# Optimization experiments

Hardware: AMD Instinct MI355X
Metric: run time of the kernel (lower is better)

## Reference

```python
import jax, jax.numpy as jnp
import numpy as np

N = 100000   # nodes
E = 1600000  # edges
G = 2048     # graphs in batch
NC = 204     # n_classes
DEPTH = 5
EPS = 1e-5


def setup_inputs() -> dict:
    key = jax.random.key(0)
    ks = jax.random.split(key, 20)
    rn = lambda k, s, sc=0.05: (jax.random.normal(k, s, jnp.float32) * sc)
    inp = {
        "h": jax.random.normal(ks[0], (N, 78), jnp.float32),
        "edge_src": jax.random.randint(ks[1], (E,), 0, N),
        "edge_dst": jax.random.randint(ks[2], (E,), 0, N),
        "graph_ids": jnp.sort(jax.random.randint(ks[3], (N,), 0, G)),
        "W1": rn(ks[4], (78, 128)),
        "b1": rn(ks[5], (128,)),
        "g1_gamma": jnp.ones((128,), jnp.float32),
        "g1_beta": jnp.zeros((128,), jnp.float32),
        "Wg": rn(ks[6], (DEPTH - 1, 128, 128)),
        "bg": rn(ks[7], (DEPTH - 1, 128)),
        "g_gamma": jnp.ones((DEPTH - 1, 128), jnp.float32),
        "g_beta": jnp.zeros((DEPTH - 1, 128), jnp.float32),
        "fc1_W": rn(ks[8], (128, 512)),
        "fc1_b": rn(ks[9], (512,)),
        "bn1_gamma": jnp.ones((512,), jnp.float32),
        "bn1_beta": jnp.zeros((512,), jnp.float32),
        "lin_W": rn(ks[10], (512, 256)),
        "lin_b": rn(ks[11], (256,)),
        "lbn_gamma": jnp.ones((256,), jnp.float32),
        "lbn_beta": jnp.zeros((256,), jnp.float32),
        "fc2_W": rn(ks[12], (256, 408)),
        "fc2_b": rn(ks[13], (408,)),
    }
    return inp


def _bn(x, gamma, beta):
    # torch BatchNorm1d training-mode normalization: biased batch var, eps=1e-5
    mu = jnp.mean(x, axis=0)
    var = jnp.var(x, axis=0)
    return (x - mu) * jax.lax.rsqrt(var + EPS) * gamma + beta


def _gin(h, src, dst, W, b):
    # DGL GINConv (eps=0, sum agg): apply_func(h + sum_neigh(h)); module adds apply_func(h)
    agg = jax.ops.segment_sum(h[src], dst, num_segments=h.shape[0])  # [N, d]
    return (h + agg) @ W + b + (h @ W + b)


def reference(h, edge_src, edge_dst, graph_ids, W1, b1, g1_gamma, g1_beta,
              Wg, bg, g_gamma, g_beta, fc1_W, fc1_b, bn1_gamma, bn1_beta,
              lin_W, lin_b, lbn_gamma, lbn_beta, fc2_W, fc2_b):
    x = jax.nn.relu(_bn(_gin(h, edge_src, edge_dst, W1, b1), g1_gamma, g1_beta))
    for i in range(DEPTH - 1):
        x = jax.nn.relu(_bn(_gin(x, edge_src, edge_dst, Wg[i], bg[i]),
                            g_gamma[i], g_beta[i]))
    # sum readout over nodes of each graph -> [G, 128]
    xg = jax.ops.segment_sum(x, graph_ids, num_segments=G)
    x = jax.nn.relu(_bn(xg @ fc1_W + fc1_b, bn1_gamma, bn1_beta))
    x = jax.nn.relu(_bn(x @ lin_W + lin_b, lbn_gamma, lbn_beta))
    logits = x @ fc2_W + fc2_b          # [G, 2*NC]
    return jax.nn.sigmoid(logits[:, -NC:])  # [G, NC]
```

## Files before the change

kernel.cpp:

```cpp
#include <hip/hip_runtime.h>
#include <hip/hip_bf16.h>
#include <math.h>

#define N_NODES 100000
#define N_EDGES 1600000
#define N_GRAPHS 2048
#define NCLS 204
#define EPS_BN 1e-5f
#define NBUCK ((N_NODES + 255) / 256)
#define BIN_CHUNK 8192

typedef __attribute__((ext_vector_type(8))) short short8;
typedef __attribute__((ext_vector_type(4))) float f32x4;

__device__ __forceinline__ float bf_lo(uint v) { union { uint i; float f; } c; c.i = v << 16; return c.f; }
__device__ __forceinline__ float bf_hi(uint v) { union { uint i; float f; } c; c.i = v & 0xffff0000u; return c.f; }
__device__ __forceinline__ ushort f2bf(float v) {
  __hip_bfloat16 b = __float2bfloat16(v);
  return *reinterpret_cast<ushort*>(&b);
}
__device__ __forceinline__ uint pack2(float a, float b) {
  return (uint)f2bf(a) | ((uint)f2bf(b) << 16);
}

__global__ __launch_bounds__(256) void k_bin_count(const int* __restrict__ dst,
                                                   int* __restrict__ bcnt, int E) {
  __shared__ int hist[NBUCK];
  int t = threadIdx.x;
  int e0 = blockIdx.x * BIN_CHUNK;
  for (int b = t; b < NBUCK; b += 256) hist[b] = 0;
  __syncthreads();
  for (int e = e0 + t; e < min(e0 + BIN_CHUNK, E); e += 256)
    atomicAdd(&hist[dst[e] >> 8], 1);
  __syncthreads();
  for (int b = t; b < NBUCK; b += 256)
    if (hist[b] > 0) atomicAdd(&bcnt[b], hist[b]);
}

__global__ __launch_bounds__(512) void k_bucket_scan(const int* __restrict__ bcnt,
                                                     int* __restrict__ bbase,
                                                     int* __restrict__ bcur) {
  __shared__ int sh[512];
  int t = threadIdx.x;
  int v = (t < NBUCK) ? bcnt[t] : 0;
  sh[t] = v;
  __syncthreads();
  for (int d = 1; d < 512; d <<= 1) {
    int x = (t >= d) ? sh[t - d] : 0;
    __syncthreads();
    sh[t] += x;
    __syncthreads();
  }
  if (t < NBUCK) {
    bbase[t + 1] = sh[t];
    bcur[t] = sh[t] - v;
    if (t == 0) bbase[0] = 0;
  }
}

__global__ __launch_bounds__(256) void k_bin(const int* __restrict__ src,
                                             const int* __restrict__ dst,
                                             int* __restrict__ cursor,
                                             uint* __restrict__ staging, int E) {
  __shared__ int hist[NBUCK];
  __shared__ int base_s[NBUCK];
  int t = threadIdx.x;
  int e0 = blockIdx.x * BIN_CHUNK;
  for (int b = t; b < NBUCK; b += 256) hist[b] = 0;
  __syncthreads();
  for (int e = e0 + t; e < min(e0 + BIN_CHUNK, E); e += 256)
    atomicAdd(&hist[dst[e] >> 8], 1);
  __syncthreads();
  for (int b = t; b < NBUCK; b += 256) {
    int hh = hist[b];
    if (hh > 0) base_s[b] = atomicAdd(&cursor[b], hh);
    hist[b] = 0;
  }
  __syncthreads();
  for (int e = e0 + t; e < min(e0 + BIN_CHUNK, E); e += 256) {
    int d = dst[e];
    int b = d >> 8;
    int r = atomicAdd(&hist[b], 1);
    staging[base_s[b] + r] = (uint)src[e] | ((uint)(d & 255) << 24);
  }
}

__global__ __launch_bounds__(256) void k_place2(const uint* __restrict__ staging,
                                                const int* __restrict__ bbase,
                                                int* __restrict__ row_ptr,
                                                int* __restrict__ csr, int nNodes, int E) {
  __shared__ int cnt[256];
  __shared__ int scn[256];
  __shared__ int cur[256];
  int t = threadIdx.x;
  int b = blockIdx.x;
  int n0 = b * 256;
  cnt[t] = 0;
  __syncthreads();
  int s = bbase[b], e = bbase[b + 1];
  for (int i = s + t; i < e; i += 256) atomicAdd(&cnt[staging[i] >> 24], 1);
  __syncthreads();
  int v = cnt[t];
  scn[t] = v;
  __syncthreads();
  for (int d = 1; d < 256; d <<= 1) {
    int x = (t >= d) ? scn[t - d] : 0;
    __syncthreads();
    scn[t] += x;
    __syncthreads();
  }
  int excl = scn[t] - v;
  if (n0 + t < nNodes) row_ptr[n0 + t] = s + excl;
  cur[t] = s + excl;
  __syncthreads();
  for (int i = s + t; i < e; i += 256) {
    uint ed = staging[i];
    int pos = atomicAdd(&cur[ed >> 24], 1);
    csr[pos] = (int)(ed & 0xFFFFFF);
  }
  if (b == 0 && t == 0) row_ptr[nNodes] = E;
}

__global__ void k_conv_h(const float* __restrict__ h, uint* __restrict__ hb, int nNodes) {
  int i = blockIdx.x * blockDim.x + threadIdx.x;
  if (i < nNodes * 64) {
    int n = i >> 6, cp = i & 63;
    int c = cp * 2;
    float a = (c < 78) ? h[(size_t)n * 78 + c] : 0.0f;
    float b = (c + 1 < 78) ? h[(size_t)n * 78 + c + 1] : 0.0f;
    hb[i] = pack2(a, b);
  }
}

__global__ void k_prep_wt_all(const float* __restrict__ W1, const float* __restrict__ Wg,
                              ushort* __restrict__ Wt) {
  int i = blockIdx.x * blockDim.x + threadIdx.x;
  int layer = blockIdx.y;
  if (i < 128 * 128) {
    int n = i >> 7, k = i & 127;
    const float* W = (layer == 0) ? W1 : Wg + (size_t)(layer - 1) * 128 * 128;
    int K = (layer == 0) ? 78 : 128;
    float v = (k < K) ? W[(size_t)k * 128 + n] : 0.0f;
    Wt[(size_t)layer * 128 * 128 + i] = f2bf(v);
  }
}

__global__ void k_prep_wt_gen(const float* __restrict__ W, int wld, int col_off, int nkeep,
                              int K, ushort* __restrict__ Wt, int total) {
  int i = blockIdx.x * blockDim.x + threadIdx.x;
  if (i < total) {
    int n = i / K, k = i - n * K;
    float v = (n < nkeep) ? W[(size_t)k * wld + col_off + n] : 0.0f;
    Wt[i] = f2bf(v);
  }
}

template <bool NRM>
__global__ __launch_bounds__(256) void k_agg_f(const uint* __restrict__ y,
                                               const int* __restrict__ row_ptr,
                                               const int* __restrict__ csr,
                                               const float* __restrict__ psum,
                                               const float* __restrict__ psq,
                                               const float* __restrict__ pgamma,
                                               const float* __restrict__ pbeta,
                                               float invM,
                                               uint* __restrict__ M, int nNodes) {
  int n = blockIdx.x * 4 + (threadIdx.x >> 6);
  if (n >= nNodes) return;
  int l = threadIdx.x & 63;
  float A0 = 1.f, B0 = 0.f, A1 = 1.f, B1 = 0.f;
  if (NRM) {
    int c0 = 2 * l, c1 = 2 * l + 1;
    float mu0 = psum[c0] * invM;
    float va0 = psq[c0] * invM - mu0 * mu0;
    A0 = pgamma[c0] * rsqrtf(va0 + EPS_BN);
    B0 = pbeta[c0] - mu0 * A0;
    float mu1 = psum[c1] * invM;
    float va1 = psq[c1] * invM - mu1 * mu1;
    A1 = pgamma[c1] * rsqrtf(va1 + EPS_BN);
    B1 = pbeta[c1] - mu1 * A1;
  }
  auto flo = [&](uint v) { float x = bf_lo(v); return NRM ? fmaxf(x * A0 + B0, 0.f) : x; };
  auto fhi = [&](uint v) { float x = bf_hi(v); return NRM ? fmaxf(x * A1 + B1, 0.f) : x; };

  uint self = y[(size_t)n * 64 + l];
  float a0 = 2.0f * flo(self);
  float a1 = 2.0f * fhi(self);
  int s = row_ptr[n], e = row_ptr[n + 1];

  for (int base = s; base < e; base += 64) {
    int cnt = e - base;
    if (cnt > 64) cnt = 64;
    int myidx = (base + l < e) ? csr[base + l] : 0;
    int j = 0;
    for (; j + 4 <= cnt; j += 4) {
      int i0 = __shfl(myidx, j);
      int i1 = __shfl(myidx, j + 1);
      int i2 = __shfl(myidx, j + 2);
      int i3 = __shfl(myidx, j + 3);
      uint v0 = y[(size_t)i0 * 64 + l];
      uint v1 = y[(size_t)i1 * 64 + l];
      uint v2 = y[(size_t)i2 * 64 + l];
      uint v3 = y[(size_t)i3 * 64 + l];
      a0 += flo(v0) + flo(v1) + flo(v2) + flo(v3);
      a1 += fhi(v0) + fhi(v1) + fhi(v2) + fhi(v3);
    }
    for (; j < cnt; j++) {
      int i0 = __shfl(myidx, j);
      uint v = y[(size_t)i0 * 64 + l];
      a0 += flo(v);
      a1 += fhi(v);
    }
  }
  M[(size_t)n * 64 + l] = pack2(a0, a1);
}

#define SWZ(row, boff) ((boff) ^ (((row) & 7) << 4))
__global__ __launch_bounds__(256) void k_gemm_mfma(const ushort* __restrict__ A,
                                                   const ushort* __restrict__ Wt,
                                                   const float* __restrict__ bias, float bscale,
                                                   ushort* __restrict__ Y, int Mrows,
                                                   float* __restrict__ gsum,
                                                   float* __restrict__ gsq) {
  __shared__ ushort As[128 * 128];
  __shared__ ushort Bs[128 * 128];
  __shared__ float sred[4][128], qred[4][128];
  int t = threadIdx.x;
  int r0 = blockIdx.x * 128;
  char* Ab = (char*)As;
  char* Bb = (char*)Bs;

  for (int it = 0; it < 8; it++) {
    int e = it * 256 + t;
    int row = e >> 4, seg = e & 15;
    uint4 va = make_uint4(0, 0, 0, 0);
    int gr = r0 + row;
    if (gr < Mrows) va = *reinterpret_cast<const uint4*>(A + (size_t)gr * 128 + seg * 8);
    *reinterpret_cast<uint4*>(Ab + row * 256 + SWZ(row, seg * 16)) = va;
    uint4 vb = *reinterpret_cast<const uint4*>(Wt + (size_t)row * 128 + seg * 8);
    *reinterpret_cast<uint4*>(Bb + row * 256 + SWZ(row, seg * 16)) = vb;
  }
  __syncthreads();

  int wi = t >> 6;
  int l = t & 63;
  int lr = l & 15;
  int kp = l >> 4;

  f32x4 acc[2][8];
#pragma unroll
  for (int mi = 0; mi < 2; mi++)
#pragma unroll
    for (int ni = 0; ni < 8; ni++) acc[mi][ni] = (f32x4){0.f, 0.f, 0.f, 0.f};

#pragma unroll
  for (int ki = 0; ki < 4; ki++) {
    short8 a[2], b[8];
#pragma unroll
    for (int mi = 0; mi < 2; mi++) {
      int row = wi * 32 + mi * 16 + lr;
      a[mi] = *reinterpret_cast<const short8*>(Ab + row * 256 + SWZ(row, ki * 64 + kp * 16));
    }
#pragma unroll
    for (int ni = 0; ni < 8; ni++) {
      int row = ni * 16 + lr;
      b[ni] = *reinterpret_cast<const short8*>(Bb + row * 256 + SWZ(row, ki * 64 + kp * 16));
    }
#pragma unroll
    for (int mi = 0; mi < 2; mi++)
#pragma unroll
      for (int ni = 0; ni < 8; ni++)
        acc[mi][ni] = __builtin_amdgcn_mfma_f32_16x16x32_bf16(a[mi], b[ni], acc[mi][ni], 0, 0, 0);
  }

  float s_part[8], q_part[8];
#pragma unroll
  for (int ni = 0; ni < 8; ni++) { s_part[ni] = 0.f; q_part[ni] = 0.f; }

#pragma unroll
  for (int mi = 0; mi < 2; mi++) {
    int rbase = r0 + wi * 32 + mi * 16 + kp * 4;
#pragma unroll
    for (int ni = 0; ni < 8; ni++) {
      int col = ni * 16 + lr;
      float bb = bscale * bias[col];
#pragma unroll
      for (int j = 0; j < 4; j++) {
        int r = rbase + j;
        if (r < Mrows) {
          float yv = acc[mi][ni][j] + bb;
          Y[(size_t)r * 128 + col] = f2bf(yv);
          s_part[ni] += yv;
          q_part[ni] += yv * yv;
        }
      }
    }
  }

#pragma unroll
  for (int ni = 0; ni < 8; ni++) {
    s_part[ni] += __shfl_xor(s_part[ni], 16, 64);
    s_part[ni] += __shfl_xor(s_part[ni], 32, 64);
    q_part[ni] += __shfl_xor(q_part[ni], 16, 64);
    q_part[ni] += __shfl_xor(q_part[ni], 32, 64);
  }
  if (kp == 0) {
#pragma unroll
    for (int ni = 0; ni < 8; ni++) {
      sred[wi][ni * 16 + lr] = s_part[ni];
      qred[wi][ni * 16 + lr] = q_part[ni];
    }
  }
  __syncthreads();
  if (t < 128) {
    float S = sred[0][t] + sred[1][t] + sred[2][t] + sred[3][t];
    float Q = qred[0][t] + qred[1][t] + qred[2][t] + qred[3][t];
    atomicAdd(&gsum[t], S);
    atomicAdd(&gsq[t], Q);
  }
}

template <int AMODE, int OMODE>
__global__ __launch_bounds__(256) void k_head_mfma(const void* __restrict__ Aptr,
                                                   int Mrows, int K,
                                                   const ushort* __restrict__ Wt,
                                                   const float* __restrict__ bias,
                                                   int col_off, int ncols,
                                                   const float* __restrict__ nAc,
                                                   const float* __restrict__ nBc,
                                                   void* __restrict__ Yout, int Nld,
                                                   float* __restrict__ gsum,
                                                   float* __restrict__ gsq) {
  __shared__ ushort As[128 * 128];
  __shared__ ushort Bs[128 * 128];
  __shared__ float sred[4][128], qred[4][128];
  int t = threadIdx.x;
  int r0 = blockIdx.y * 128;
  int c0 = blockIdx.x * 128;
  char* Ab = (char*)As;
  char* Bb = (char*)Bs;

  int wi = t >> 6;
  int l = t & 63;
  int lr = l & 15;
  int kp = l >> 4;

  f32x4 acc[2][8];
#pragma unroll
  for (int mi = 0; mi < 2; mi++)
#pragma unroll
    for (int ni = 0; ni < 8; ni++) acc[mi][ni] = (f32x4){0.f, 0.f, 0.f, 0.f};

  for (int k0 = 0; k0 < K; k0 += 128) {
    if (k0) __syncthreads();
    for (int it = 0; it < 8; it++) {
      int e = it * 256 + t;
      int row = e >> 4, seg = e & 15;
      int gr = r0 + row;
      uint4 va;
      if (AMODE == 0) {
        const float* Af = (const float*)Aptr;
        float4 f0 = {0.f, 0.f, 0.f, 0.f}, f1 = {0.f, 0.f, 0.f, 0.f};
        if (gr < Mrows) {
          f0 = *reinterpret_cast<const float4*>(Af + (size_t)gr * K + k0 + seg * 8);
          f1 = *reinterpret_cast<const float4*>(Af + (size_t)gr * K + k0 + seg * 8 + 4);
        }
        va.x = pack2(f0.x, f0.y); va.y = pack2(f0.z, f0.w);
        va.z = pack2(f1.x, f1.y); va.w = pack2(f1.z, f1.w);
      } else {
        const uint* Au = (const uint*)Aptr;
        uint4 r4 = make_uint4(0, 0, 0, 0);
        if (gr < Mrows) r4 = *reinterpret_cast<const uint4*>(Au + (size_t)gr * (K >> 1) + ((k0 + seg * 8) >> 1));
        int c = k0 + seg * 8;
        uint uu[4] = {r4.x, r4.y, r4.z, r4.w};
#pragma unroll
        for (int q = 0; q < 4; q++) {
          float aa = fmaxf(bf_lo(uu[q]) * nAc[c + 2 * q] + nBc[c + 2 * q], 0.f);
          float bb = fmaxf(bf_hi(uu[q]) * nAc[c + 2 * q + 1] + nBc[c + 2 * q + 1], 0.f);
          uu[q] = pack2(aa, bb);
        }
        va = make_uint4(uu[0], uu[1], uu[2], uu[3]);
      }
      *reinterpret_cast<uint4*>(Ab + row * 256 + SWZ(row, seg * 16)) = va;
      uint4 vb = *reinterpret_cast<const uint4*>(Wt + (size_t)(c0 + row) * K + k0 + seg * 8);
      *reinterpret_cast<uint4*>(Bb + row * 256 + SWZ(row, seg * 16)) = vb;
    }
    __syncthreads();

#pragma unroll
    for (int ki = 0; ki < 4; ki++) {
      short8 a[2], b[8];
#pragma unroll
      for (int mi = 0; mi < 2; mi++) {
        int row = wi * 32 + mi * 16 + lr;
        a[mi] = *reinterpret_cast<const short8*>(Ab + row * 256 + SWZ(row, ki * 64 + kp * 16));
      }
#pragma unroll
      for (int ni = 0; ni < 8; ni++) {
        int row = ni * 16 + lr;
        b[ni] = *reinterpret_cast<const short8*>(Bb + row * 256 + SWZ(row, ki * 64 + kp * 16));
      }
#pragma unroll
      for (int mi = 0; mi < 2; mi++)
#pragma unroll
        for (int ni = 0; ni < 8; ni++)
          acc[mi][ni] = __builtin_amdgcn_mfma_f32_16x16x32_bf16(a[mi], b[ni], acc[mi][ni], 0, 0, 0);
    }
  }

  if (OMODE == 0) {
    float s_part[8], q_part[8];
#pragma unroll
    for (int ni = 0; ni < 8; ni++) { s_part[ni] = 0.f; q_part[ni] = 0.f; }
#pragma unroll
    for (int mi = 0; mi < 2; mi++) {
      int rbase = r0 + wi * 32 + mi * 16 + kp * 4;
#pragma unroll
      for (int ni = 0; ni < 8; ni++) {
        int gc = c0 + ni * 16 + lr;
        float bb = bias[col_off + gc];
#pragma unroll
        for (int j = 0; j < 4; j++) {
          int r = rbase + j;
          if (r < Mrows) {
            float yv = acc[mi][ni][j] + bb;
            ((ushort*)Yout)[(size_t)r * Nld + gc] = f2bf(yv);
            s_part[ni] += yv;
            q_part[ni] += yv * yv;
          }
        }
      }
    }
#pragma unroll
    for (int ni = 0; ni < 8; ni++) {
      s_part[ni] += __shfl_xor(s_part[ni], 16, 64);
      s_part[ni] += __shfl_xor(s_part[ni], 32, 64);
      q_part[ni] += __shfl_xor(q_part[ni], 16, 64);
      q_part[ni] += __shfl_xor(q_part[ni], 32, 64);
    }
    if (kp == 0) {
#pragma unroll
      for (int ni = 0; ni < 8; ni++) {
        sred[wi][ni * 16 + lr] = s_part[ni];
        qred[wi][ni * 16 + lr] = q_part[ni];
      }
    }
    __syncthreads();
    if (t < 128) {
      float S = sred[0][t] + sred[1][t] + sred[2][t] + sred[3][t];
      float Q = qred[0][t] + qred[1][t] + qred[2][t] + qred[3][t];
      atomicAdd(&gsum[c0 + t], S);
      atomicAdd(&gsq[c0 + t], Q);
    }
  } else {
#pragma unroll
    for (int mi = 0; mi < 2; mi++) {
      int rbase = r0 + wi * 32 + mi * 16 + kp * 4;
#pragma unroll
      for (int ni = 0; ni < 8; ni++) {
        int gc = c0 + ni * 16 + lr;
        if (gc < ncols) {
          float bb = bias[col_off + gc];
#pragma unroll
          for (int j = 0; j < 4; j++) {
            int r = rbase + j;
            if (r < Mrows) {
              float v = acc[mi][ni][j] + bb;
              ((float*)Yout)[(size_t)r * Nld + gc] = 1.0f / (1.0f + expf(-v));
            }
          }
        }
      }
    }
  }
}

__global__ void k_bnparams(const float* __restrict__ sum, const float* __restrict__ sumsq,
                           const float* __restrict__ gamma, const float* __restrict__ beta,
                           float* __restrict__ Ac, float* __restrict__ Bc,
                           int C, float invM) {
  int c = blockIdx.x * blockDim.x + threadIdx.x;
  if (c < C) {
    float mu = sum[c] * invM;
    float var = sumsq[c] * invM - mu * mu;
    float rs = rsqrtf(var + EPS_BN);
    float a = gamma[c] * rs;
    Ac[c] = a;
    Bc[c] = beta[c] - mu * a;
  }
}

__global__ __launch_bounds__(64) void k_readout(const uint* __restrict__ y,
                                                const int* __restrict__ gid,
                                                const float* __restrict__ psum,
                                                const float* __restrict__ psq,
                                                const float* __restrict__ pgamma,
                                                const float* __restrict__ pbeta,
                                                float invM,
                                                float* __restrict__ xg, int nNodes) {
  int l = threadIdx.x;
  int n0 = blockIdx.x * 64;
  int n1 = min(n0 + 64, nNodes);
  if (n0 >= nNodes) return;
  int c0 = 2 * l, c1 = 2 * l + 1;
  float mu0 = psum[c0] * invM;
  float va0 = psq[c0] * invM - mu0 * mu0;
  float A0 = pgamma[c0] * rsqrtf(va0 + EPS_BN);
  float B0 = pbeta[c0] - mu0 * A0;
  float mu1 = psum[c1] * invM;
  float va1 = psq[c1] * invM - mu1 * mu1;
  float A1 = pgamma[c1] * rsqrtf(va1 + EPS_BN);
  float B1 = pbeta[c1] - mu1 * A1;
  float a0 = 0, a1 = 0;
  int cur = gid[n0];
  for (int n = n0; n < n1; n++) {
    int g = gid[n];
    if (g != cur) {
      atomicAdd(&xg[(size_t)cur * 128 + 2 * l], a0);
      atomicAdd(&xg[(size_t)cur * 128 + 2 * l + 1], a1);
      a0 = 0; a1 = 0; cur = g;
    }
    uint v = y[(size_t)n * 64 + l];
    a0 += fmaxf(bf_lo(v) * A0 + B0, 0.f);
    a1 += fmaxf(bf_hi(v) * A1 + B1, 0.f);
  }
  atomicAdd(&xg[(size_t)cur * 128 + 2 * l], a0);
  atomicAdd(&xg[(size_t)cur * 128 + 2 * l + 1], a1);
}

extern "C" void kernel_launch(void* const* d_in, const int* in_sizes, int n_in,
                              void* d_out, int out_size, void* d_ws, size_t ws_size,
                              hipStream_t stream) {
  const float* h    = (const float*)d_in[0];
  const int*   esrc = (const int*)d_in[1];
  const int*   edst = (const int*)d_in[2];
  const int*   gid  = (const int*)d_in[3];
  const float* W1   = (const float*)d_in[4];
  const float* b1   = (const float*)d_in[5];
  const float* g1g  = (const float*)d_in[6];
  const float* g1b  = (const float*)d_in[7];
  const float* Wg   = (const float*)d_in[8];
  const float* bg   = (const float*)d_in[9];
  const float* gg   = (const float*)d_in[10];
  const float* gb   = (const float*)d_in[11];
  const float* fc1W = (const float*)d_in[12];
  const float* fc1b = (const float*)d_in[13];
  const float* bn1g = (const float*)d_in[14];
  const float* bn1b = (const float*)d_in[15];
  const float* linW = (const float*)d_in[16];
  const float* linb = (const float*)d_in[17];
  const float* lbng = (const float*)d_in[18];
  const float* lbnb = (const float*)d_in[19];
  const float* fc2W = (const float*)d_in[20];
  const float* fc2b = (const float*)d_in[21];
  float* out = (float*)d_out;

  char* p = (char*)d_ws;
  auto alloc = [&](size_t bytes) {
    char* q = p;
    p += (bytes + 255) & ~(size_t)255;
    return q;
  };
  int* row_ptr = (int*)alloc((N_NODES + 1) * sizeof(int));
  int* bcnt    = (int*)alloc(NBUCK * sizeof(int));
  int* bbase   = (int*)alloc((NBUCK + 1) * sizeof(int));
  int* bcur    = (int*)alloc(NBUCK * sizeof(int));
  int* csr     = (int*)alloc(N_EDGES * sizeof(int));
  uint* hb     = (uint*)alloc((size_t)N_NODES * 64 * sizeof(uint));
  uint* Mb     = (uint*)alloc((size_t)N_NODES * 64 * sizeof(uint));
  uint* yb     = (uint*)alloc((size_t)N_NODES * 64 * sizeof(uint));
  ushort* Wt   = (ushort*)alloc(5 * 128 * 128 * sizeof(ushort));
  ushort* fc1Wt = (ushort*)alloc(512 * 128 * sizeof(ushort));
  ushort* linWt = (ushort*)alloc(256 * 512 * sizeof(ushort));
  ushort* fc2Wt = (ushort*)alloc(256 * 256 * sizeof(ushort));
  float* stats = (float*)alloc(2816 * sizeof(float));
  float* Ac    = (float*)alloc(512 * sizeof(float));
  float* Bc    = (float*)alloc(512 * sizeof(float));
  float* xg    = (float*)alloc((size_t)N_GRAPHS * 128 * sizeof(float));
  uint* y1b    = (uint*)alloc((size_t)N_GRAPHS * 256 * sizeof(uint));
  uint* y2b    = (uint*)alloc((size_t)N_GRAPHS * 128 * sizeof(uint));
  uint* staging = (uint*)Mb;

  float* lsum = stats;
  float* fsum1 = stats + 1280;
  float* fsq1  = stats + 1792;
  float* lsum2 = stats + 2304;
  float* lsq2  = stats + 2560;

  k_conv_h<<<(N_NODES * 64 + 255) / 256, 256, 0, stream>>>(h, hb, N_NODES);
  {
    dim3 g(64, 5);
    k_prep_wt_all<<<g, 256, 0, stream>>>(W1, Wg, Wt);
  }
  k_prep_wt_gen<<<(512 * 128 + 255) / 256, 256, 0, stream>>>(fc1W, 512, 0, 512, 128, fc1Wt, 512 * 128);
  k_prep_wt_gen<<<(256 * 512 + 255) / 256, 256, 0, stream>>>(linW, 256, 0, 256, 512, linWt, 256 * 512);
  k_prep_wt_gen<<<(256 * 256 + 255) / 256, 256, 0, stream>>>(fc2W, 408, 204, 204, 256, fc2Wt, 256 * 256);

  hipMemsetAsync(stats, 0, 2816 * sizeof(float), stream);
  hipMemsetAsync(xg, 0, (size_t)N_GRAPHS * 128 * sizeof(float), stream);

  hipMemsetAsync(bcnt, 0, NBUCK * sizeof(int), stream);
  k_bin_count<<<(N_EDGES + BIN_CHUNK - 1) / BIN_CHUNK, 256, 0, stream>>>(edst, bcnt, N_EDGES);
  k_bucket_scan<<<1, 512, 0, stream>>>(bcnt, bbase, bcur);
  k_bin<<<(N_EDGES + BIN_CHUNK - 1) / BIN_CHUNK, 256, 0, stream>>>(esrc, edst, bcur,
                                                                   staging, N_EDGES);
  k_place2<<<NBUCK, 256, 0, stream>>>(staging, bbase, row_ptr, csr, N_NODES, N_EDGES);

  const float invN = 1.0f / (float)N_NODES;
  const float invG = 1.0f / (float)N_GRAPHS;

  for (int layer = 0; layer < 5; layer++) {
    const ushort* Wl = Wt + (size_t)layer * 128 * 128;
    const float* bl  = (layer == 0) ? b1 : bg + (size_t)(layer - 1) * 128;
    const float* pg  = (layer == 1) ? g1g : gg + (size_t)(layer - 2) * 128;
    const float* pb  = (layer == 1) ? g1b : gb + (size_t)(layer - 2) * 128;
    float* st = lsum + (size_t)layer * 256;

    if (layer == 0)
      k_agg_f<false><<<(N_NODES + 3) / 4, 256, 0, stream>>>(hb, row_ptr, csr,
                                                            nullptr, nullptr, nullptr, nullptr,
                                                            invN, Mb, N_NODES);
    else
      k_agg_f<true><<<(N_NODES + 3) / 4, 256, 0, stream>>>(yb, row_ptr, csr,
                                                           lsum + (size_t)(layer - 1) * 256,
                                                           lsum + (size_t)(layer - 1) * 256 + 128,
                                                           pg, pb, invN, Mb, N_NODES);
    k_gemm_mfma<<<(N_NODES + 127) / 128, 256, 0, stream>>>((const ushort*)Mb, Wl, bl, 2.0f,
                                                           (ushort*)yb, N_NODES,
                                                           st, st + 128);
  }

  k_readout<<<(N_NODES + 63) / 64, 64, 0, stream>>>(yb, gid,
                                                    lsum + 4 * 256, lsum + 4 * 256 + 128,
                                                    gg + 3 * 128, gb + 3 * 128, invN,
                                                    xg, N_NODES);

  k_head_mfma<0, 0><<<dim3(4, 16), 256, 0, stream>>>(xg, N_GRAPHS, 128, fc1Wt, fc1b, 0, 512,
                                                     nullptr, nullptr, y1b, 512, fsum1, fsq1);
  k_bnparams<<<1, 512, 0, stream>>>(fsum1, fsq1, bn1g, bn1b, Ac, Bc, 512, invG);

  k_head_mfma<1, 0><<<dim3(2, 16), 256, 0, stream>>>(y1b, N_GRAPHS, 512, linWt, linb, 0, 256,
                                                     Ac, Bc, y2b, 256, lsum2, lsq2);
  k_bnparams<<<1, 256, 0, stream>>>(lsum2, lsq2, lbng, lbnb, Ac, Bc, 256, invG);

  k_head_mfma<1, 1><<<dim3(2, 16), 256, 0, stream>>>(y2b, N_GRAPHS, 256, fc2Wt, fc2b, 204, NCLS,
                                                     Ac, Bc, out, NCLS, nullptr, nullptr);
}
```

Before: 651.6 us.

## Switch activations to fp16 and gather 16-byte rows across wave slots

After: 682.3 us. 1.05x slower.

```diff
diff --git a/kernel.cpp b/kernel.cpp
--- a/kernel.cpp
+++ b/kernel.cpp
@@ -1,5 +1,5 @@
 #include <hip/hip_runtime.h>
-#include <hip/hip_bf16.h>
+#include <hip/hip_fp16.h>
 #include <math.h>
 
 #define N_NODES 100000
@@ -10,17 +10,20 @@
 #define NBUCK ((N_NODES + 255) / 256)
 #define BIN_CHUNK 8192
 
-typedef __attribute__((ext_vector_type(8))) short short8;
+typedef __attribute__((ext_vector_type(8))) _Float16 f16x8;
 typedef __attribute__((ext_vector_type(4))) float f32x4;
 
-__device__ __forceinline__ float bf_lo(uint v) { union { uint i; float f; } c; c.i = v << 16; return c.f; }
-__device__ __forceinline__ float bf_hi(uint v) { union { uint i; float f; } c; c.i = v & 0xffff0000u; return c.f; }
-__device__ __forceinline__ ushort f2bf(float v) {
-  __hip_bfloat16 b = __float2bfloat16(v);
-  return *reinterpret_cast<ushort*>(&b);
-}
-__device__ __forceinline__ uint pack2(float a, float b) {
-  return (uint)f2bf(a) | ((uint)f2bf(b) << 16);
+__device__ __forceinline__ uint pack2h(float a, float b) {
+  __half2 h = __floats2half2_rn(a, b);
+  return *reinterpret_cast<uint*>(&h);
+}
+__device__ __forceinline__ float2 unpack2h(uint u) {
+  __half2 h = *reinterpret_cast<__half2*>(&u);
+  return __half22float2(h);
+}
+__device__ __forceinline__ ushort f2h(float v) {
+  __half h = __float2half_rn(v);
+  return *reinterpret_cast<ushort*>(&h);
 }
 
 __global__ __launch_bounds__(256) void k_bin_count(const int* __restrict__ dst,
@@ -88,7 +91,7 @@
 __global__ __launch_bounds__(256) void k_place2(const uint* __restrict__ staging,
                                                 const int* __restrict__ bbase,
                                                 int* __restrict__ row_ptr,
-                                                int* __restrict__ csr, int nNodes, int E) {
+                                                uint* __restrict__ csrb, int nNodes, int E) {
   __shared__ int cnt[256];
   __shared__ int scn[256];
   __shared__ int cur[256];
@@ -116,7 +119,7 @@
   for (int i = s + t; i < e; i += 256) {
     uint ed = staging[i];
     int pos = atomicAdd(&cur[ed >> 24], 1);
-    csr[pos] = (int)(ed & 0xFFFFFF);
+    csrb[pos] = (ed & 0xFFFFFF) << 8;
   }
   if (b == 0 && t == 0) row_ptr[nNodes] = E;
 }
@@ -128,7 +131,7 @@
     int c = cp * 2;
     float a = (c < 78) ? h[(size_t)n * 78 + c] : 0.0f;
     float b = (c + 1 < 78) ? h[(size_t)n * 78 + c + 1] : 0.0f;
-    hb[i] = pack2(a, b);
+    hb[i] = pack2h(a, b);
   }
 }
 
@@ -141,7 +144,7 @@
     const float* W = (layer == 0) ? W1 : Wg + (size_t)(layer - 1) * 128 * 128;
     int K = (layer == 0) ? 78 : 128;
     float v = (k < K) ? W[(size_t)k * 128 + n] : 0.0f;
-    Wt[(size_t)layer * 128 * 128 + i] = f2bf(v);
+    Wt[(size_t)layer * 128 * 128 + i] = f2h(v);
   }
 }
 
@@ -151,68 +154,102 @@
   if (i < total) {
     int n = i / K, k = i - n * K;
     float v = (n < nkeep) ? W[(size_t)k * wld + col_off + n] : 0.0f;
-    Wt[i] = f2bf(v);
+    Wt[i] = f2h(v);
   }
 }
 
 template <bool NRM>
-__global__ __launch_bounds__(256) void k_agg_f(const uint* __restrict__ y,
+__global__ __launch_bounds__(256) void k_agg_f(const char* __restrict__ xraw,
                                                const int* __restrict__ row_ptr,
-                                               const int* __restrict__ csr,
+                                               const uint* __restrict__ csrb,
                                                const float* __restrict__ psum,
                                                const float* __restrict__ psq,
                                                const float* __restrict__ pgamma,
                                                const float* __restrict__ pbeta,
                                                float invM,
-                                               uint* __restrict__ M, int nNodes) {
+                                               char* __restrict__ Mraw, int nNodes) {
   int n = blockIdx.x * 4 + (threadIdx.x >> 6);
   if (n >= nNodes) return;
   int l = threadIdx.x & 63;
-  float A0 = 1.f, B0 = 0.f, A1 = 1.f, B1 = 0.f;
+  int slot = l >> 4;
+  int ch16 = l & 15;
+  int coff = ch16 * 16;
+
+  float Ap[8], Bp[8];
   if (NRM) {
-    int c0 = 2 * l, c1 = 2 * l + 1;
-    float mu0 = psum[c0] * invM;
-    float va0 = psq[c0] * invM - mu0 * mu0;
-    A0 = pgamma[c0] * rsqrtf(va0 + EPS_BN);
-    B0 = pbeta[c0] - mu0 * A0;
-    float mu1 = psum[c1] * invM;
-    float va1 = psq[c1] * invM - mu1 * mu1;
-    A1 = pgamma[c1] * rsqrtf(va1 + EPS_BN);
-    B1 = pbeta[c1] - mu1 * A1;
-  }
-  auto flo = [&](uint v) { float x = bf_lo(v); return NRM ? fmaxf(x * A0 + B0, 0.f) : x; };
-  auto fhi = [&](uint v) { float x = bf_hi(v); return NRM ? fmaxf(x * A1 + B1, 0.f) : x; };
-
-  uint self = y[(size_t)n * 64 + l];
-  float a0 = 2.0f * flo(self);
-  float a1 = 2.0f * fhi(self);
+    int c0 = ch16 * 8;
+    float4 s0 = *reinterpret_cast<const float4*>(psum + c0);
+    float4 s1 = *reinterpret_cast<const float4*>(psum + c0 + 4);
+    float4 q0 = *reinterpret_cast<const float4*>(psq + c0);
+    float4 q1 = *reinterpret_cast<const float4*>(psq + c0 + 4);
+    float4 g0 = *reinterpret_cast<const float4*>(pgamma + c0);
+    float4 g1 = *reinterpret_cast<const float4*>(pgamma + c0 + 4);
+    float4 b0 = *reinterpret_cast<const float4*>(pbeta + c0);
+    float4 b1 = *reinterpret_cast<const float4*>(pbeta + c0 + 4);
+    float sv[8] = {s0.x, s0.y, s0.z, s0.w, s1.x, s1.y, s1.z, s1.w};
+    float qv[8] = {q0.x, q0.y, q0.z, q0.w, q1.x, q1.y, q1.z, q1.w};
+    float gv[8] = {g0.x, g0.y, g0.z, g0.w, g1.x, g1.y, g1.z, g1.w};
+    float bv[8] = {b0.x, b0.y, b0.z, b0.w, b1.x, b1.y, b1.z, b1.w};
+#pragma unroll
+    for (int k = 0; k < 8; k++) {
+      float mu = sv[k] * invM;
+      float var = qv[k] * invM - mu * mu;
+      Ap[k] = gv[k] * rsqrtf(var + EPS_BN);
+      Bp[k] = bv[k] - mu * Ap[k];
+    }
+  }
+
+  float acc[8];
+#pragma unroll
+  for (int k = 0; k < 8; k++) acc[k] = 0.f;
+
+  auto accum = [&](uint4 v, float w) {
+    float2 f0 = unpack2h(v.x), f1 = unpack2h(v.y), f2 = unpack2h(v.z), f3 = unpack2h(v.w);
+    float f[8] = {f0.x, f0.y, f1.x, f1.y, f2.x, f2.y, f3.x, f3.y};
+#pragma unroll
+    for (int k = 0; k < 8; k++) {
+      float x = NRM ? fmaxf(f[k] * Ap[k] + Bp[k], 0.f) : f[k];
+      acc[k] += w * x;
+    }
+  };
+
+  if (slot == 0) {
+    uint4 v = *reinterpret_cast<const uint4*>(xraw + (size_t)n * 256 + coff);
+    accum(v, 2.0f);
+  }
+
   int s = row_ptr[n], e = row_ptr[n + 1];
-
   for (int base = s; base < e; base += 64) {
     int cnt = e - base;
     if (cnt > 64) cnt = 64;
-    int myidx = (base + l < e) ? csr[base + l] : 0;
-    int j = 0;
-    for (; j + 4 <= cnt; j += 4) {
-      int i0 = __shfl(myidx, j);
-      int i1 = __shfl(myidx, j + 1);
-      int i2 = __shfl(myidx, j + 2);
-      int i3 = __shfl(myidx, j + 3);
-      uint v0 = y[(size_t)i0 * 64 + l];
-      uint v1 = y[(size_t)i1 * 64 + l];
-      uint v2 = y[(size_t)i2 * 64 + l];
-      uint v3 = y[(size_t)i3 * 64 + l];
-      a0 += flo(v0) + flo(v1) + flo(v2) + flo(v3);
-      a1 += fhi(v0) + fhi(v1) + fhi(v2) + fhi(v3);
-    }
-    for (; j < cnt; j++) {
-      int i0 = __shfl(myidx, j);
-      uint v = y[(size_t)i0 * 64 + l];
-      a0 += flo(v);
-      a1 += fhi(v);
-    }
-  }
-  M[(size_t)n * 64 + l] = pack2(a0, a1);
+    uint myoff = (base + l < e) ? csrb[base + l] : 0;
+    int nfull = cnt >> 2;
+    for (int j = 0; j < nfull; j++) {
+      uint off = __shfl(myoff, 4 * j + slot);
+      uint4 v = *reinterpret_cast<const uint4*>(xraw + (size_t)off + coff);
+      accum(v, 1.0f);
+    }
+    int jj = nfull * 4 + slot;
+    uint off = __shfl(myoff, jj < 64 ? jj : 63);
+    if (jj < cnt) {
+      uint4 v = *reinterpret_cast<const uint4*>(xraw + (size_t)off + coff);
+      accum(v, 1.0f);
+    }
+  }
+
+#pragma unroll
+  for (int k = 0; k < 8; k++) {
+    acc[k] += __shfl_xor(acc[k], 16);
+    acc[k] += __shfl_xor(acc[k], 32);
+  }
+  if (slot == 0) {
+    uint4 o;
+    o.x = pack2h(acc[0], acc[1]);
+    o.y = pack2h(acc[2], acc[3]);
+    o.z = pack2h(acc[4], acc[5]);
+    o.w = pack2h(acc[6], acc[7]);
+    *reinterpret_cast<uint4*>(Mraw + (size_t)n * 256 + coff) = o;
+  }
 }
 
 #define SWZ(row, boff) ((boff) ^ (((row) & 7) << 4))
@@ -255,22 +292,22 @@
 
 #pragma unroll
   for (int ki = 0; ki < 4; ki++) {
-    short8 a[2], b[8];
+    f16x8 a[2], b[8];
 #pragma unroll
     for (int mi = 0; mi < 2; mi++) {
       int row = wi * 32 + mi * 16 + lr;
-      a[mi] = *reinterpret_cast<const short8*>(Ab + row * 256 + SWZ(row, ki * 64 + kp * 16));
+      a[mi] = *reinterpret_cast<const f16x8*>(Ab + row * 256 + SWZ(row, ki * 64 + kp * 16));
     }
 #pragma unroll
     for (int ni = 0; ni < 8; ni++) {
       int row = ni * 16 + lr;
-      b[ni] = *reinterpret_cast<const short8*>(Bb + row * 256 + SWZ(row, ki * 64 + kp * 16));
+      b[ni] = *reinterpret_cast<const f16x8*>(Bb + row * 256 + SWZ(row, ki * 64 + kp * 16));
     }
 #pragma unroll
     for (int mi = 0; mi < 2; mi++)
 #pragma unroll
       for (int ni = 0; ni < 8; ni++)
-        acc[mi][ni] = __builtin_amdgcn_mfma_f32_16x16x32_bf16(a[mi], b[ni], acc[mi][ni], 0, 0, 0);
+        acc[mi][ni] = __builtin_amdgcn_mfma_f32_16x16x32_f16(a[mi], b[ni], acc[mi][ni], 0, 0, 0);
   }
 
   float s_part[8], q_part[8];
@@ -289,7 +326,7 @@
         int r = rbase + j;
         if (r < Mrows) {
           float yv = acc[mi][ni][j] + bb;
-          Y[(size_t)r * 128 + col] = f2bf(yv);
+          Y[(size_t)r * 128 + col] = f2h(yv);
           s_part[ni] += yv;
           q_part[ni] += yv * yv;
         }
@@ -365,8 +402,8 @@
           f0 = *reinterpret_cast<const float4*>(Af + (size_t)gr * K + k0 + seg * 8);
           f1 = *reinterpret_cast<const float4*>(Af + (size_t)gr * K + k0 + seg * 8 + 4);
         }
-        va.x = pack2(f0.x, f0.y); va.y = pack2(f0.z, f0.w);
-        va.z = pack2(f1.x, f1.y); va.w = pack2(f1.z, f1.w);
+        va.x = pack2h(f0.x, f0.y); va.y = pack2h(f0.z, f0.w);
+        va.z = pack2h(f1.x, f1.y); va.w = pack2h(f1.z, f1.w);
       } else {
         const uint* Au = (const uint*)Aptr;
         uint4 r4 = make_uint4(0, 0, 0, 0);
@@ -375,9 +412,10 @@
         uint uu[4] = {r4.x, r4.y, r4.z, r4.w};
 #pragma unroll
         for (int q = 0; q < 4; q++) {
-          float aa = fmaxf(bf_lo(uu[q]) * nAc[c + 2 * q] + nBc[c + 2 * q], 0.f);
-          float bb = fmaxf(bf_hi(uu[q]) * nAc[c + 2 * q + 1] + nBc[c + 2 * q + 1], 0.f);
-          uu[q] = pack2(aa, bb);
+          float2 f = unpack2h(uu[q]);
+          float aa = fmaxf(f.x * nAc[c + 2 * q] + nBc[c + 2 * q], 0.f);
+          float bb = fmaxf(f.y * nAc[c + 2 * q + 1] + nBc[c + 2 * q + 1], 0.f);
+          uu[q] = pack2h(aa, bb);
         }
         va = make_uint4(uu[0], uu[1], uu[2], uu[3]);
       }
@@ -389,22 +427,22 @@
 
 #pragma unroll
     for (int ki = 0; ki < 4; ki++) {
-      short8 a[2], b[8];
+      f16x8 a[2], b[8];
 #pragma unroll
       for (int mi = 0; mi < 2; mi++) {
         int row = wi * 32 + mi * 16 + lr;
-        a[mi] = *reinterpret_cast<const short8*>(Ab + row * 256 + SWZ(row, ki * 64 + kp * 16));
+        a[mi] = *reinterpret_cast<const f16x8*>(Ab + row * 256 + SWZ(row, ki * 64 + kp * 16));
       }
 #pragma unroll
       for (int ni = 0; ni < 8; ni++) {
         int row = ni * 16 + lr;
-        b[ni] = *reinterpret_cast<const short8*>(Bb + row * 256 + SWZ(row, ki * 64 + kp * 16));
+        b[ni] = *reinterpret_cast<const f16x8*>(Bb + row * 256 + SWZ(row, ki * 64 + kp * 16));
       }
 #pragma unroll
       for (int mi = 0; mi < 2; mi++)
 #pragma unroll
         for (int ni = 0; ni < 8; ni++)
-          acc[mi][ni] = __builtin_amdgcn_mfma_f32_16x16x32_bf16(a[mi], b[ni], acc[mi][ni], 0, 0, 0);
+          acc[mi][ni] = __builtin_amdgcn_mfma_f32_16x16x32_f16(a[mi], b[ni], acc[mi][ni], 0, 0, 0);
     }
   }
 
@@ -424,7 +462,7 @@
           int r = rbase + j;
           if (r < Mrows) {
             float yv = acc[mi][ni][j] + bb;
-            ((ushort*)Yout)[(size_t)r * Nld + gc] = f2bf(yv);
+            ((ushort*)Yout)[(size_t)r * Nld + gc] = f2h(yv);
             s_part[ni] += yv;
             q_part[ni] += yv * yv;
           }
@@ -520,9 +558,9 @@
       atomicAdd(&xg[(size_t)cur * 128 + 2 * l + 1], a1);
       a0 = 0; a1 = 0; cur = g;
     }
-    uint v = y[(size_t)n * 64 + l];
-    a0 += fmaxf(bf_lo(v) * A0 + B0, 0.f);
-    a1 += fmaxf(bf_hi(v) * A1 + B1, 0.f);
+    float2 f = unpack2h(y[(size_t)n * 64 + l]);
+    a0 += fmaxf(f.x * A0 + B0, 0.f);
+    a1 += fmaxf(f.y * A1 + B1, 0.f);
   }
   atomicAdd(&xg[(size_t)cur * 128 + 2 * l], a0);
   atomicAdd(&xg[(size_t)cur * 128 + 2 * l + 1], a1);
@@ -565,7 +603,7 @@
   int* bcnt    = (int*)alloc(NBUCK * sizeof(int));
   int* bbase   = (int*)alloc((NBUCK + 1) * sizeof(int));
   int* bcur    = (int*)alloc(NBUCK * sizeof(int));
-  int* csr     = (int*)alloc(N_EDGES * sizeof(int));
+  uint* csrb   = (uint*)alloc(N_EDGES * sizeof(uint));
   uint* hb     = (uint*)alloc((size_t)N_NODES * 64 * sizeof(uint));
   uint* Mb     = (uint*)alloc((size_t)N_NODES * 64 * sizeof(uint));
   uint* yb     = (uint*)alloc((size_t)N_NODES * 64 * sizeof(uint));
@@ -604,7 +642,7 @@
   k_bucket_scan<<<1, 512, 0, stream>>>(bcnt, bbase, bcur);
   k_bin<<<(N_EDGES + BIN_CHUNK - 1) / BIN_CHUNK, 256, 0, stream>>>(esrc, edst, bcur,
                                                                    staging, N_EDGES);
-  k_place2<<<NBUCK, 256, 0, stream>>>(staging, bbase, row_ptr, csr, N_NODES, N_EDGES);
+  k_place2<<<NBUCK, 256, 0, stream>>>(staging, bbase, row_ptr, csrb, N_NODES, N_EDGES);
 
   const float invN = 1.0f / (float)N_NODES;
   const float invG = 1.0f / (float)N_GRAPHS;
@@ -617,14 +655,14 @@
     float* st = lsum + (size_t)layer * 256;
 
     if (layer == 0)
-      k_agg_f<false><<<(N_NODES + 3) / 4, 256, 0, stream>>>(hb, row_ptr, csr,
+      k_agg_f<false><<<(N_NODES + 3) / 4, 256, 0, stream>>>((const char*)hb, row_ptr, csrb,
                                                             nullptr, nullptr, nullptr, nullptr,
-                                                            invN, Mb, N_NODES);
+                                                            invN, (char*)Mb, N_NODES);
     else
-      k_agg_f<true><<<(N_NODES + 3) / 4, 256, 0, stream>>>(yb, row_ptr, csr,
+      k_agg_f<true><<<(N_NODES + 3) / 4, 256, 0, stream>>>((const char*)yb, row_ptr, csrb,
                                                            lsum + (size_t)(layer - 1) * 256,
                                                            lsum + (size_t)(layer - 1) * 256 + 128,
-                                                           pg, pb, invN, Mb, N_NODES);
+                                                           pg, pb, invN, (char*)Mb, N_NODES);
     k_gemm_mfma<<<(N_NODES + 127) / 128, 256, 0, stream>>>((const ushort*)Mb, Wl, bl, 2.0f,
                                                            (ushort*)yb, N_NODES,
                                                            st, st + 128);
```
